# Kernel optimization log

Hardware: AMD Instinct MI355X
Metric: run time of the kernel (lower is better)

The kernel has to match this reference:

```python
import jax, jax.numpy as jnp
import numpy as np

N, B, D, H, E = 1024, 8, 768, 8, 16384
DH = D // H
EPS = 1e-5


def setup_inputs() -> dict:
    key = jax.random.key(0)
    ks = jax.random.split(key, 12)
    s = 0.02
    return {
        "x": jax.random.normal(ks[0], (N, B, D), jnp.float32),
        "edge_index": jax.random.randint(ks[1], (B, 2, E), 0, N, jnp.int32),
        "gcn_W": jax.random.normal(ks[2], (D, D), jnp.float32) * s,
        "gcn_b": jnp.zeros((D,), jnp.float32),
        "in_proj_w": jax.random.normal(ks[3], (3 * D, D), jnp.float32) * s,
        "in_proj_b": jnp.zeros((3 * D,), jnp.float32),
        "out_proj_w": jax.random.normal(ks[4], (D, D), jnp.float32) * s,
        "out_proj_b": jnp.zeros((D,), jnp.float32),
        "gate_w": jax.random.normal(ks[5], (D, 2 * D), jnp.float32) * s,
        "gate_b": jnp.zeros((D,), jnp.float32),
        "ln_g": jnp.ones((D,), jnp.float32),
        "ln_b": jnp.zeros((D,), jnp.float32),
    }


def _gcn(xb, edge_index, gcn_W, gcn_b):
    # xb: [B, N, D] node features; edge_index: [B, 2, E]
    h = xb @ gcn_W.T  # linear first, as in PyG GCNConv
    loops = jnp.arange(N, dtype=edge_index.dtype)

    def agg(h_b, ei_b):
        src = jnp.concatenate([ei_b[0], loops])  # add self-loops
        dst = jnp.concatenate([ei_b[1], loops])
        deg = jax.ops.segment_sum(jnp.ones_like(src, h_b.dtype), dst, num_segments=N)
        dinv = jnp.where(deg > 0, jax.lax.rsqrt(deg), 0.0)
        norm = dinv[src] * dinv[dst]  # symmetric normalization
        msg = norm[:, None] * h_b[src]
        return jax.ops.segment_sum(msg, dst, num_segments=N)

    return jax.vmap(agg)(h, edge_index) + gcn_b  # [B, N, D]


def _mha(x, in_proj_w, in_proj_b, out_proj_w, out_proj_b):
    # x: [N, B, D] (seq-first, as nn.MultiheadAttention default)
    qkv = x @ in_proj_w.T + in_proj_b  # [N, B, 3D]
    q, k, v = jnp.split(qkv, 3, axis=-1)

    def heads(t):  # [N, B, D] -> [B, H, N, DH]
        return t.reshape(N, B, H, DH).transpose(1, 2, 0, 3)

    q, k, v = heads(q), heads(k), heads(v)
    scores = jnp.einsum("bhqd,bhkd->bhqk", q, k) / jnp.sqrt(jnp.float32(DH))
    attn = jax.nn.softmax(scores, axis=-1)
    ctx = jnp.einsum("bhqk,bhkd->bhqd", attn, v)  # [B, H, N, DH]
    ctx = ctx.transpose(2, 0, 1, 3).reshape(N, B, D)
    return ctx @ out_proj_w.T + out_proj_b


def _layernorm(x, g, b):
    mu = jnp.mean(x, axis=-1, keepdims=True)
    var = jnp.mean(jnp.square(x - mu), axis=-1, keepdims=True)
    return (x - mu) * jax.lax.rsqrt(var + EPS) * g + b


def reference(x, edge_index, gcn_W, gcn_b, in_proj_w, in_proj_b,
              out_proj_w, out_proj_b, gate_w, gate_b, ln_g, ln_b):
    xb = x.transpose(1, 0, 2)  # [B, N, D]
    gcn_out = _gcn(xb, edge_index, gcn_W, gcn_b).transpose(1, 0, 2)  # [N, B, D]
    attn_out = _mha(x, in_proj_w, in_proj_b, out_proj_w, out_proj_b)  # [N, B, D]
    combined = jnp.concatenate([gcn_out, attn_out], axis=-1)
    gate = jax.nn.sigmoid(combined @ gate_w.T + gate_b)
    fused = gate * gcn_out + (1.0 - gate) * attn_out
    return _layernorm(fused + x, ln_g, ln_b)
```

## Files before the change

### kernel.cpp

```cpp
#include <hip/hip_runtime.h>


typedef __attribute__((ext_vector_type(8))) short b16x8;
typedef __attribute__((ext_vector_type(4))) float f32x4;

using gu32 = __attribute__((address_space(1))) const unsigned int;
using lu32 = __attribute__((address_space(3))) unsigned int;

constexpr int N  = 1024;
constexpr int B  = 8;
constexpr int D  = 768;
constexpr int H  = 8;
constexpr int DH = 96;
constexpr int E  = 16384;
constexpr int M  = N * B;
constexpr float LN_EPS = 1e-5f;

#define DEV static __device__ __forceinline__

DEV unsigned short f2b(float f) {
  unsigned u = __float_as_uint(f);
  u += 0x7fffu + ((u >> 16) & 1u);
  return (unsigned short)(u >> 16);
}
DEV float b2f(unsigned short h) { return __uint_as_float(((unsigned)h) << 16); }

__global__ void cast_f2b_kernel(const float* __restrict__ in,
                                unsigned short* __restrict__ out, int n4) {
  int i = blockIdx.x * 256 + threadIdx.x;
  if (i < n4) {
    float4 v = ((const float4*)in)[i];
    ushort4 o;
    o.x = f2b(v.x); o.y = f2b(v.y); o.z = f2b(v.z); o.w = f2b(v.w);
    ((ushort4*)out)[i] = o;
  }
}

__global__ void zero_i32_kernel(int* __restrict__ p, int n) {
  int i = blockIdx.x * 256 + threadIdx.x;
  if (i < n) p[i] = 0;
}

__global__ void edge_count_kernel(const int* __restrict__ ei, int* __restrict__ cnt) {
  int i = blockIdx.x * 256 + threadIdx.x;
  int b = i >> 14, e = i & (E - 1);
  int dst = ei[(b << 15) + E + e];
  atomicAdd(&cnt[(b << 10) + dst], 1);
}

__global__ __launch_bounds__(1024) void scan_offs_kernel(
    const int* __restrict__ cnt, int* __restrict__ offs,
    int* __restrict__ cursor, float* __restrict__ dinv) {
  __shared__ int buf[1024];
  const int b = blockIdx.x, i = threadIdx.x, g = (b << 10) + i;
  const int c = cnt[g];
  buf[i] = c;
  __syncthreads();
  for (int off = 1; off < 1024; off <<= 1) {
    int t = (i >= off) ? buf[i - off] : 0;
    __syncthreads();
    buf[i] += t;
    __syncthreads();
  }
  const int excl = buf[i] - c;
  offs[g] = excl;
  cursor[g] = excl;
  dinv[g] = rsqrtf((float)(c + 1));
}

__global__ void edge_fill_kernel(const int* __restrict__ ei,
                                 int* __restrict__ cursor, int* __restrict__ elist) {
  int i = blockIdx.x * 256 + threadIdx.x;
  int b = i >> 14, e = i & (E - 1);
  int src = ei[(b << 15) + e];
  int dst = ei[(b << 15) + E + e];
  int slot = atomicAdd(&cursor[(b << 10) + dst], 1);
  elist[(b << 14) + slot] = src;
}

constexpr int EPI_FUSED = 0;
constexpr int EPI_ATTN  = 1;
constexpr int EPI_GATE  = 2;

template <int EPI, int BN, int K>
__global__ __launch_bounds__(256) void gemm_bt(
    const unsigned short* __restrict__ A, const unsigned short* __restrict__ W,
    const float* __restrict__ bias,
    void* __restrict__ p0, void* __restrict__ p1, void* __restrict__ p2,
    void* __restrict__ p3) {
  constexpr int NW = BN / 32;
  constexpr int NT = K / 32;
  __shared__ __align__(16) unsigned short sA[2][128][32];
  __shared__ __align__(16) unsigned short sB[2][BN][32];
  const int tid = threadIdx.x;
  const int lane = tid & 63, wid = tid >> 6;
  const int wm = wid >> 1, wn = wid & 1;
  const int m0 = blockIdx.y * 128, n0 = blockIdx.x * BN;
  const int l15 = lane & 15, lhi = lane >> 4;
  const int srow = lane >> 2, scol = (lane & 3) * 8;

  f32x4 acc[4][NW] = {};

  const unsigned short* pa = A + ((size_t)(m0 + wid * 32 + srow)) * K + scol;
  const unsigned short* pb = W + ((size_t)(n0 + wid * (BN / 4) + srow)) * K + scol;

  auto stage = [&](int buf) {
    __builtin_amdgcn_global_load_lds((gu32*)pa, (lu32*)&sA[buf][wid * 32][0], 16, 0, 0);
    __builtin_amdgcn_global_load_lds((gu32*)(pa + 16 * K),
                                     (lu32*)&sA[buf][wid * 32 + 16][0], 16, 0, 0);
    __builtin_amdgcn_global_load_lds((gu32*)pb, (lu32*)&sB[buf][wid * (BN / 4)][0], 16, 0, 0);
    if constexpr (BN == 128)
      __builtin_amdgcn_global_load_lds((gu32*)(pb + 16 * K),
                                       (lu32*)&sB[buf][wid * 32 + 16][0], 16, 0, 0);
    pa += 32; pb += 32;
  };

  stage(0);
  int cur = 0;
  for (int kt = 0; kt < NT; ++kt) {
    if (kt + 1 < NT) {
      stage(cur ^ 1);
      if constexpr (BN == 128) asm volatile("s_waitcnt vmcnt(4)" ::: "memory");
      else                     asm volatile("s_waitcnt vmcnt(3)" ::: "memory");
    } else {
      asm volatile("s_waitcnt vmcnt(0)" ::: "memory");
    }
    __builtin_amdgcn_s_barrier();
    __builtin_amdgcn_sched_barrier(0);

    b16x8 af[4], bfr[NW];
#pragma unroll
    for (int i = 0; i < 4; ++i)
      af[i] = *(const b16x8*)&sA[cur][wm * 64 + i * 16 + l15][lhi * 8];
#pragma unroll
    for (int j = 0; j < NW; ++j)
      bfr[j] = *(const b16x8*)&sB[cur][wn * (BN / 2) + j * 16 + l15][lhi * 8];
#pragma unroll
    for (int i = 0; i < 4; ++i)
#pragma unroll
      for (int j = 0; j < NW; ++j)
        acc[i][j] = __builtin_amdgcn_mfma_f32_16x16x32_bf16(af[i], bfr[j], acc[i][j], 0, 0, 0);

    __builtin_amdgcn_sched_barrier(0);
    __builtin_amdgcn_s_barrier();
    cur ^= 1;
  }

#pragma unroll
  for (int i = 0; i < 4; ++i) {
#pragma unroll
    for (int j = 0; j < NW; ++j) {
      const int c = n0 + wn * (BN / 2) + j * 16 + l15;
      float bv;
      if constexpr (EPI == EPI_FUSED) bv = (c < 768) ? 0.0f : bias[c - 768];
      else bv = bias[c];
#pragma unroll
      for (int g = 0; g < 4; ++g) {
        const int r = m0 + wm * 64 + i * 16 + lhi * 4 + g;
        float v = acc[i][j][g] + bv;
        if constexpr (EPI == EPI_FUSED) {
          const int n = r >> 3, b = r & 7;
          if (c < 768) {
            ((unsigned short*)p0)[((size_t)((b << 10) + n)) * 768 + c] = f2b(v);
          } else {
            const int cc2 = c - 768;
            const int sec = cc2 / 768, cc = cc2 - sec * 768;
            const int hd = cc / 96, dh = cc - hd * 96;
            unsigned short* dst =
                (sec == 0) ? (unsigned short*)p1
                           : (sec == 1 ? (unsigned short*)p2 : (unsigned short*)p3);
            size_t idx;
            if (sec < 2) idx = ((size_t)((b * 8 + hd) * 1024 + n)) * 96 + dh;
            else         idx = ((size_t)((b * 8 + hd) * 96 + dh)) * 1024 + n;
            dst[idx] = f2b(v);
          }
        } else if constexpr (EPI == EPI_ATTN) {
          ((float*)p1)[(size_t)r * 768 + c] = v;
          ((unsigned short*)p0)[(size_t)r * 1536 + 768 + c] = f2b(v);
        } else {
          ((float*)p1)[(size_t)r * 768 + c] = 1.0f / (1.0f + __expf(-v));
        }
      }
    }
  }
}

__global__ __launch_bounds__(256) void attn_kernel(
    const unsigned short* __restrict__ qb, const unsigned short* __restrict__ kb,
    const unsigned short* __restrict__ vb, unsigned short* __restrict__ ctx) {
  __shared__ __align__(16) unsigned short sK[64][104];
  __shared__ __align__(16) unsigned short sV[96][72];
  __shared__ __align__(16) unsigned short sP[4][16][72];
  const int tid = threadIdx.x, lane = tid & 63, wid = tid >> 6;
  const int l15 = lane & 15, lhi = lane >> 4;
  const int bid = blockIdx.x;
  const int xcd = bid & 7, slot = bid >> 3;
  const int bh = xcd * 8 + (slot >> 4);
  const int q0 = (slot & 15) * 64;
  const float SCL = 0.14724445f;

  b16x8 qf[3];
  const size_t qbase = ((size_t)bh * 1024 + q0 + wid * 16 + l15) * 96 + lhi * 8;
#pragma unroll
  for (int ks = 0; ks < 3; ++ks) qf[ks] = *(const b16x8*)(qb + qbase + ks * 32);

  const int c0 = tid, c1 = 256 + tid, c2 = 512 + tid;
  const unsigned short* kp0 = kb + ((size_t)bh * 1024 + c0 / 12) * 96 + (c0 % 12) * 8;
  const unsigned short* kp1 = kb + ((size_t)bh * 1024 + c1 / 12) * 96 + (c1 % 12) * 8;
  const unsigned short* kp2 = kb + ((size_t)bh * 1024 + c2 / 12) * 96 + (c2 % 12) * 8;
  const unsigned short* vp0 = vb + ((size_t)bh * 96 + (c0 >> 3)) * 1024 + (c0 & 7) * 8;
  const unsigned short* vp1 = vb + ((size_t)bh * 96 + (c1 >> 3)) * 1024 + (c1 & 7) * 8;
  const unsigned short* vp2 = vb + ((size_t)bh * 96 + (c2 >> 3)) * 1024 + (c2 & 7) * 8;
  unsigned short* sk0 = &sK[c0 / 12][(c0 % 12) * 8];
  unsigned short* sk1 = &sK[c1 / 12][(c1 % 12) * 8];
  unsigned short* sk2 = &sK[c2 / 12][(c2 % 12) * 8];
  unsigned short* sv0 = &sV[c0 >> 3][(c0 & 7) * 8];
  unsigned short* sv1 = &sV[c1 >> 3][(c1 & 7) * 8];
  unsigned short* sv2 = &sV[c2 >> 3][(c2 & 7) * 8];

  uint4 k0 = *(const uint4*)kp0, k1 = *(const uint4*)kp1, k2 = *(const uint4*)kp2;
  uint4 v0 = *(const uint4*)vp0, v1 = *(const uint4*)vp1, v2 = *(const uint4*)vp2;

  f32x4 accO[6] = {};
  float ssum[4] = {0.f, 0.f, 0.f, 0.f};

  for (int kt = 0; kt < 16; ++kt) {
    __syncthreads();
    *(uint4*)sk0 = k0; *(uint4*)sk1 = k1; *(uint4*)sk2 = k2;
    *(uint4*)sv0 = v0; *(uint4*)sv1 = v1; *(uint4*)sv2 = v2;
    __syncthreads();
    if (kt < 15) {
      kp0 += 64 * 96; kp1 += 64 * 96; kp2 += 64 * 96;
      vp0 += 64;      vp1 += 64;      vp2 += 64;
      k0 = *(const uint4*)kp0; k1 = *(const uint4*)kp1; k2 = *(const uint4*)kp2;
      v0 = *(const uint4*)vp0; v1 = *(const uint4*)vp1; v2 = *(const uint4*)vp2;
    }

    f32x4 sf[4] = {};
#pragma unroll
    for (int f = 0; f < 4; ++f) {
#pragma unroll
      for (int ks = 0; ks < 3; ++ks) {
        b16x8 kf = *(const b16x8*)&sK[f * 16 + l15][ks * 32 + lhi * 8];
        sf[f] = __builtin_amdgcn_mfma_f32_16x16x32_bf16(qf[ks], kf, sf[f], 0, 0, 0);
      }
    }

#pragma unroll
    for (int g = 0; g < 4; ++g) {
#pragma unroll
      for (int f = 0; f < 4; ++f) {
        const float pv = exp2f(sf[f][g] * SCL);
        sP[wid][lhi * 4 + g][f * 16 + l15] = f2b(pv);
        ssum[g] += pv;
      }
    }

#pragma unroll
    for (int ks = 0; ks < 2; ++ks) {
      b16x8 pa = *(const b16x8*)&sP[wid][l15][ks * 32 + lhi * 8];
#pragma unroll
      for (int o = 0; o < 6; ++o) {
        b16x8 vf = *(const b16x8*)&sV[o * 16 + l15][ks * 32 + lhi * 8];
        accO[o] = __builtin_amdgcn_mfma_f32_16x16x32_bf16(pa, vf, accO[o], 0, 0, 0);
      }
    }
  }

#pragma unroll
  for (int g = 0; g < 4; ++g) {
#pragma unroll
    for (int msk = 1; msk < 16; msk <<= 1) ssum[g] += __shfl_xor(ssum[g], msk);
  }

  const int b = bh >> 3, hd = bh & 7;
  float rinv[4];
#pragma unroll
  for (int g = 0; g < 4; ++g) rinv[g] = 1.0f / ssum[g];
#pragma unroll
  for (int o = 0; o < 6; ++o)
#pragma unroll
    for (int g = 0; g < 4; ++g) {
      const int qrow = q0 + wid * 16 + lhi * 4 + g;
      ctx[((size_t)qrow * 8 + b) * 768 + hd * 96 + o * 16 + l15] =
          f2b(accO[o][g] * rinv[g]);
    }
}

__global__ __launch_bounds__(192) void gcn_agg_kernel(
    const unsigned short* __restrict__ h16,
    const int* __restrict__ cnt, const int* __restrict__ offs,
    const int* __restrict__ elist, const float* __restrict__ dinv,
    const float* __restrict__ gcn_b, float* __restrict__ gcn_f32,
    unsigned short* __restrict__ cat16) {
  const int bn = blockIdx.x;
  const int b = bn >> 10, n = bn & 1023;
  const int d = threadIdx.x * 4;
  const float dn = dinv[bn];
  const size_t hrow = (size_t)bn * 768;
  ushort4 hv = *(const ushort4*)(h16 + hrow + d);
  float a0 = dn * dn * b2f(hv.x), a1 = dn * dn * b2f(hv.y);
  float a2 = dn * dn * b2f(hv.z), a3 = dn * dn * b2f(hv.w);
  const int st = offs[bn], cv = cnt[bn];
  const int* ep = elist + (b << 14) + st;
  int src = (cv > 0) ? ep[0] : 0;
  for (int i = 0; i < cv; ++i) {
    const int nsrc = (i + 1 < cv) ? ep[i + 1] : 0;
    const float nv = dinv[(b << 10) + src] * dn;
    const ushort4 sv = *(const ushort4*)(h16 + ((size_t)((b << 10) + src)) * 768 + d);
    a0 += nv * b2f(sv.x); a1 += nv * b2f(sv.y);
    a2 += nv * b2f(sv.z); a3 += nv * b2f(sv.w);
    src = nsrc;
  }
  const float4 bb = *(const float4*)(gcn_b + d);
  a0 += bb.x; a1 += bb.y; a2 += bb.z; a3 += bb.w;
  *(float4*)(gcn_f32 + hrow + d) = make_float4(a0, a1, a2, a3);
  const size_t crow = ((size_t)n * 8 + b) * 1536;
  ushort4 co; co.x = f2b(a0); co.y = f2b(a1); co.z = f2b(a2); co.w = f2b(a3);
  *(ushort4*)(cat16 + crow + d) = co;
}

__global__ __launch_bounds__(192) void ln_fuse_kernel(
    const float* __restrict__ gate, const float* __restrict__ gcn,
    const float* __restrict__ attn, const float* __restrict__ x,
    const float* __restrict__ lng, const float* __restrict__ lnb,
    float* __restrict__ out) {
  const int r = blockIdx.x;
  const int t = threadIdx.x, lane = t & 63, wid = t >> 6;
  const int b = r & 7, n = r >> 3;
  const int d = t * 4;
  const size_t xrow = (size_t)r * 768;
  const size_t grow = (size_t)((b << 10) + n) * 768;
  const float4 gv = *(const float4*)(gate + xrow + d);
  const float4 cv = *(const float4*)(gcn + grow + d);
  const float4 av = *(const float4*)(attn + xrow + d);
  const float4 xv = *(const float4*)(x + xrow + d);
  float f0 = gv.x * cv.x + (1.f - gv.x) * av.x + xv.x;
  float f1 = gv.y * cv.y + (1.f - gv.y) * av.y + xv.y;
  float f2 = gv.z * cv.z + (1.f - gv.z) * av.z + xv.z;
  float f3 = gv.w * cv.w + (1.f - gv.w) * av.w + xv.w;
  float s1 = f0 + f1 + f2 + f3;
  float s2 = f0 * f0 + f1 * f1 + f2 * f2 + f3 * f3;
#pragma unroll
  for (int msk = 1; msk < 64; msk <<= 1) {
    s1 += __shfl_xor(s1, msk);
    s2 += __shfl_xor(s2, msk);
  }
  __shared__ float p1[3], p2[3];
  if (lane == 0) { p1[wid] = s1; p2[wid] = s2; }
  __syncthreads();
  s1 = p1[0] + p1[1] + p1[2];
  s2 = p2[0] + p2[1] + p2[2];
  const float mu = s1 * (1.f / 768.f);
  float var = s2 * (1.f / 768.f) - mu * mu;
  var = fmaxf(var, 0.f);
  const float rstd = rsqrtf(var + LN_EPS);
  const float4 lg = *(const float4*)(lng + d);
  const float4 lb = *(const float4*)(lnb + d);
  float4 o;
  o.x = (f0 - mu) * rstd * lg.x + lb.x;
  o.y = (f1 - mu) * rstd * lg.y + lb.y;
  o.z = (f2 - mu) * rstd * lg.z + lb.z;
  o.w = (f3 - mu) * rstd * lg.w + lb.w;
  *(float4*)(out + xrow + d) = o;
}

extern "C" void kernel_launch(void* const* d_in, const int* in_sizes, int n_in,
                              void* d_out, int out_size, void* d_ws, size_t ws_size,
                              hipStream_t stream) {
  const float* x     = (const float*)d_in[0];
  const int*   ei    = (const int*)d_in[1];
  const float* gcnW  = (const float*)d_in[2];
  const float* gcnb  = (const float*)d_in[3];
  const float* ipw   = (const float*)d_in[4];
  const float* ipb   = (const float*)d_in[5];
  const float* opw   = (const float*)d_in[6];
  const float* opb   = (const float*)d_in[7];
  const float* gw    = (const float*)d_in[8];
  const float* gb    = (const float*)d_in[9];
  const float* lng   = (const float*)d_in[10];
  const float* lnb   = (const float*)d_in[11];
  float* out = (float*)d_out;

  char* p = (char*)d_ws;
  auto alloc = [&](size_t bytes) { void* q = p; p += (bytes + 255) & ~(size_t)255; return q; };

  unsigned short* xb16  = (unsigned short*)alloc((size_t)M * 768 * 2);
  unsigned short* wcat  = (unsigned short*)alloc((size_t)3072 * 768 * 2);
  unsigned short* wout  = (unsigned short*)alloc((size_t)768 * 768 * 2);
  unsigned short* wgate = (unsigned short*)alloc((size_t)768 * 1536 * 2);
  unsigned short* qb    = (unsigned short*)alloc((size_t)B * H * N * DH * 2);
  unsigned short* kb    = (unsigned short*)alloc((size_t)B * H * N * DH * 2);
  unsigned short* vb    = (unsigned short*)alloc((size_t)B * H * DH * N * 2);
  unsigned short* h16   = (unsigned short*)alloc((size_t)M * 768 * 2);
  unsigned short* cat16 = (unsigned short*)alloc((size_t)M * 1536 * 2);
  float* gcnf           = (float*)alloc((size_t)M * 768 * 4);
  int* cnt    = (int*)alloc(8192 * 4);
  int* offs   = (int*)alloc(8192 * 4);
  int* cursor = (int*)alloc(8192 * 4);
  float* dinv = (float*)alloc(8192 * 4);
  int* elist  = (int*)alloc((size_t)B * E * 4);

  unsigned short* ctx16 = xb16;
  float* gatef = (float*)qb;
  float* attnf = (float*)vb;

  cast_f2b_kernel<<<(M * 768 / 4 + 255) / 256, 256, 0, stream>>>(x, xb16, M * 768 / 4);
  cast_f2b_kernel<<<(768 * 768 / 4 + 255) / 256, 256, 0, stream>>>(gcnW, wcat, 768 * 768 / 4);
  cast_f2b_kernel<<<(2304 * 768 / 4 + 255) / 256, 256, 0, stream>>>(
      ipw, wcat + (size_t)768 * 768, 2304 * 768 / 4);
  cast_f2b_kernel<<<(768 * 768 / 4 + 255) / 256, 256, 0, stream>>>(opw, wout, 768 * 768 / 4);
  cast_f2b_kernel<<<(768 * 1536 / 4 + 255) / 256, 256, 0, stream>>>(gw, wgate, 768 * 1536 / 4);

  zero_i32_kernel<<<32, 256, 0, stream>>>(cnt, 8192);
  edge_count_kernel<<<(B * E) / 256, 256, 0, stream>>>(ei, cnt);
  scan_offs_kernel<<<8, 1024, 0, stream>>>(cnt, offs, cursor, dinv);
  edge_fill_kernel<<<(B * E) / 256, 256, 0, stream>>>(ei, cursor, elist);

  gemm_bt<EPI_FUSED, 128, 768><<<dim3(24, 64), 256, 0, stream>>>(
      xb16, wcat, ipb, (void*)h16, (void*)qb, (void*)kb, (void*)vb);
  attn_kernel<<<1024, 256, 0, stream>>>(qb, kb, vb, ctx16);
  gcn_agg_kernel<<<8192, 192, 0, stream>>>(h16, cnt, offs, elist, dinv, gcnb,
                                           gcnf, cat16);
  gemm_bt<EPI_ATTN, 64, 768><<<dim3(12, 64), 256, 0, stream>>>(
      ctx16, wout, opb, (void*)cat16, (void*)attnf, nullptr, nullptr);
  gemm_bt<EPI_GATE, 64, 1536><<<dim3(12, 64), 256, 0, stream>>>(
      cat16, wgate, gb, nullptr, (void*)gatef, nullptr, nullptr);

  ln_fuse_kernel<<<8192, 192, 0, stream>>>(gatef, gcnf, attnf, x, lng, lnb, out);
}
```

Before: 285.1 us.

## Replace fused QKV/GCN GEMM with 256x256-tile, 8-wave pipelined kernel

Adds a dedicated 256x256-tile, 512-thread GEMM for the fused GCN-linear plus QKV projection (M=8192, N=3072, K=768). It uses K=64 double-buffered LDS stages and splits each stage into four MFMA phases, with async global-to-LDS loads interleaved between phases and s_setprio raised around the MFMA blocks. The larger tile raises arithmetic intensity and cuts redundant global traffic compared with the old 128x128 tiles. The cost is heavy register use (128 accumulator floats per lane) and only 384 blocks, which may leave the GPU's CUs unevenly loaded.

```diff
diff --git a/kernel.cpp b/kernel.cpp
--- a/kernel.cpp
+++ b/kernel.cpp
@@ -17,6 +17,7 @@
 constexpr float LN_EPS = 1e-5f;
 
 #define DEV static __device__ __forceinline__
+#define GLOAD(SRC, DST) __builtin_amdgcn_global_load_lds((gu32*)(SRC), (lu32*)(DST), 16, 0, 0)
 
 DEV unsigned short f2b(float f) {
   unsigned u = __float_as_uint(f);
@@ -78,7 +79,166 @@
   elist[(b << 14) + slot] = src;
 }
 
-constexpr int EPI_FUSED = 0;
+__global__ __launch_bounds__(512, 2) void gemm_fused256(
+    const unsigned short* __restrict__ A, const unsigned short* __restrict__ W,
+    const float* __restrict__ bias,
+    void* __restrict__ p0, void* __restrict__ p1, void* __restrict__ p2,
+    void* __restrict__ p3) {
+  __shared__ __align__(16) unsigned short sA[2][2][256][32];
+  __shared__ __align__(16) unsigned short sB[2][2][256][32];
+  const int tid = threadIdx.x;
+  const int lane = tid & 63, wid = tid >> 6;
+  const int wm = wid >> 2, wn = wid & 3;
+  const int m0 = blockIdx.y * 256, n0 = blockIdx.x * 256;
+  const int l15 = lane & 15, lhi = lane >> 4;
+
+  f32x4 acc[8][4] = {};
+
+  const unsigned short* pa = A + ((size_t)(m0 + (tid >> 2))) * 768 + (tid & 3) * 8;
+  const unsigned short* pb = W + ((size_t)(n0 + (tid >> 2))) * 768 + (tid & 3) * 8;
+  constexpr size_t RSTRIDE = (size_t)128 * 768;
+
+  GLOAD(pb,                 &sB[0][0][wid * 16][0]);
+  GLOAD(pb + RSTRIDE,       &sB[0][0][128 + wid * 16][0]);
+  GLOAD(pa,                 &sA[0][0][wid * 16][0]);
+  GLOAD(pa + RSTRIDE,       &sA[0][0][128 + wid * 16][0]);
+  GLOAD(pb + 32,            &sB[0][1][wid * 16][0]);
+  GLOAD(pb + 32 + RSTRIDE,  &sB[0][1][128 + wid * 16][0]);
+  GLOAD(pa + 32,            &sA[0][1][wid * 16][0]);
+  GLOAD(pa + 32 + RSTRIDE,  &sA[0][1][128 + wid * 16][0]);
+  asm volatile("s_waitcnt vmcnt(4)" ::: "memory");
+  __builtin_amdgcn_s_barrier();
+
+  for (int t = 0; t < 12; ++t) {
+    const int p = t & 1;
+    const bool stg = (t < 11);
+    const int kn = (t + 1) * 64;
+    b16x8 af[4], bf[4];
+
+#pragma unroll
+    for (int cf = 0; cf < 4; ++cf)
+      bf[cf] = *(const b16x8*)&sB[p][0][wn * 64 + cf * 16 + l15][lhi * 8];
+#pragma unroll
+    for (int rf = 0; rf < 4; ++rf)
+      af[rf] = *(const b16x8*)&sA[p][0][wm * 128 + rf * 16 + l15][lhi * 8];
+    if (stg) {
+      GLOAD(pb + kn,           &sB[p ^ 1][0][wid * 16][0]);
+      GLOAD(pb + kn + RSTRIDE, &sB[p ^ 1][0][128 + wid * 16][0]);
+    }
+    __builtin_amdgcn_sched_barrier(0);
+    __builtin_amdgcn_s_barrier();
+    asm volatile("s_waitcnt lgkmcnt(0)" ::: "memory");
+    __builtin_amdgcn_sched_barrier(0);
+    __builtin_amdgcn_s_setprio(1);
+#pragma unroll
+    for (int rf = 0; rf < 4; ++rf)
+#pragma unroll
+      for (int cf = 0; cf < 4; ++cf)
+        acc[rf][cf] = __builtin_amdgcn_mfma_f32_16x16x32_bf16(af[rf], bf[cf], acc[rf][cf], 0, 0, 0);
+    __builtin_amdgcn_s_setprio(0);
+    __builtin_amdgcn_sched_barrier(0);
+    __builtin_amdgcn_s_barrier();
+
+#pragma unroll
+    for (int rf = 0; rf < 4; ++rf)
+      af[rf] = *(const b16x8*)&sA[p][0][wm * 128 + 64 + rf * 16 + l15][lhi * 8];
+    if (stg) {
+      GLOAD(pa + kn,           &sA[p ^ 1][0][wid * 16][0]);
+      GLOAD(pa + kn + RSTRIDE, &sA[p ^ 1][0][128 + wid * 16][0]);
+    }
+    __builtin_amdgcn_sched_barrier(0);
+    if (stg) asm volatile("s_waitcnt vmcnt(4)" ::: "memory");
+    else     asm volatile("s_waitcnt vmcnt(0)" ::: "memory");
+    __builtin_amdgcn_s_barrier();
+    asm volatile("s_waitcnt lgkmcnt(0)" ::: "memory");
+    __builtin_amdgcn_sched_barrier(0);
+    __builtin_amdgcn_s_setprio(1);
+#pragma unroll
+    for (int rf = 0; rf < 4; ++rf)
+#pragma unroll
+      for (int cf = 0; cf < 4; ++cf)
+        acc[4 + rf][cf] = __builtin_amdgcn_mfma_f32_16x16x32_bf16(af[rf], bf[cf], acc[4 + rf][cf], 0, 0, 0);
+    __builtin_amdgcn_s_setprio(0);
+    __builtin_amdgcn_sched_barrier(0);
+    __builtin_amdgcn_s_barrier();
+
+#pragma unroll
+    for (int cf = 0; cf < 4; ++cf)
+      bf[cf] = *(const b16x8*)&sB[p][1][wn * 64 + cf * 16 + l15][lhi * 8];
+#pragma unroll
+    for (int rf = 0; rf < 4; ++rf)
+      af[rf] = *(const b16x8*)&sA[p][1][wm * 128 + rf * 16 + l15][lhi * 8];
+    if (stg) {
+      GLOAD(pb + kn + 32,           &sB[p ^ 1][1][wid * 16][0]);
+      GLOAD(pb + kn + 32 + RSTRIDE, &sB[p ^ 1][1][128 + wid * 16][0]);
+    }
+    __builtin_amdgcn_sched_barrier(0);
+    __builtin_amdgcn_s_barrier();
+    asm volatile("s_waitcnt lgkmcnt(0)" ::: "memory");
+    __builtin_amdgcn_sched_barrier(0);
+    __builtin_amdgcn_s_setprio(1);
+#pragma unroll
+    for (int rf = 0; rf < 4; ++rf)
+#pragma unroll
+      for (int cf = 0; cf < 4; ++cf)
+        acc[rf][cf] = __builtin_amdgcn_mfma_f32_16x16x32_bf16(af[rf], bf[cf], acc[rf][cf], 0, 0, 0);
+    __builtin_amdgcn_s_setprio(0);
+    __builtin_amdgcn_sched_barrier(0);
+    __builtin_amdgcn_s_barrier();
+
+#pragma unroll
+    for (int rf = 0; rf < 4; ++rf)
+      af[rf] = *(const b16x8*)&sA[p][1][wm * 128 + 64 + rf * 16 + l15][lhi * 8];
+    if (stg) {
+      GLOAD(pa + kn + 32,           &sA[p ^ 1][1][wid * 16][0]);
+      GLOAD(pa + kn + 32 + RSTRIDE, &sA[p ^ 1][1][128 + wid * 16][0]);
+    }
+    __builtin_amdgcn_sched_barrier(0);
+    if (stg) asm volatile("s_waitcnt vmcnt(4)" ::: "memory");
+    __builtin_amdgcn_s_barrier();
+    asm volatile("s_waitcnt lgkmcnt(0)" ::: "memory");
+    __builtin_amdgcn_sched_barrier(0);
+    __builtin_amdgcn_s_setprio(1);
+#pragma unroll
+    for (int rf = 0; rf < 4; ++rf)
+#pragma unroll
+      for (int cf = 0; cf < 4; ++cf)
+        acc[4 + rf][cf] = __builtin_amdgcn_mfma_f32_16x16x32_bf16(af[rf], bf[cf], acc[4 + rf][cf], 0, 0, 0);
+    __builtin_amdgcn_s_setprio(0);
+    __builtin_amdgcn_sched_barrier(0);
+    __builtin_amdgcn_s_barrier();
+  }
+
+#pragma unroll
+  for (int rg = 0; rg < 8; ++rg) {
+#pragma unroll
+    for (int cf = 0; cf < 4; ++cf) {
+      const int c = n0 + wn * 64 + cf * 16 + l15;
+      const float bv = (c < 768) ? 0.0f : bias[c - 768];
+#pragma unroll
+      for (int g = 0; g < 4; ++g) {
+        const int r = m0 + wm * 128 + rg * 16 + lhi * 4 + g;
+        float v = acc[rg][cf][g] + bv;
+        const int n = r >> 3, b = r & 7;
+        if (c < 768) {
+          ((unsigned short*)p0)[((size_t)((b << 10) + n)) * 768 + c] = f2b(v);
+        } else {
+          const int cc2 = c - 768;
+          const int sec = cc2 / 768, cc = cc2 - sec * 768;
+          const int hd = cc / 96, dh = cc - hd * 96;
+          unsigned short* dst =
+              (sec == 0) ? (unsigned short*)p1
+                         : (sec == 1 ? (unsigned short*)p2 : (unsigned short*)p3);
+          size_t idx;
+          if (sec < 2) idx = ((size_t)((b * 8 + hd) * 1024 + n)) * 96 + dh;
+          else         idx = ((size_t)((b * 8 + hd) * 96 + dh)) * 1024 + n;
+          dst[idx] = f2b(v);
+        }
+      }
+    }
+  }
+}
+
 constexpr int EPI_ATTN  = 1;
 constexpr int EPI_GATE  = 2;
 
@@ -86,8 +246,7 @@
 __global__ __launch_bounds__(256) void gemm_bt(
     const unsigned short* __restrict__ A, const unsigned short* __restrict__ W,
     const float* __restrict__ bias,
-    void* __restrict__ p0, void* __restrict__ p1, void* __restrict__ p2,
-    void* __restrict__ p3) {
+    void* __restrict__ p0, void* __restrict__ p1) {
   constexpr int NW = BN / 32;
   constexpr int NT = K / 32;
   __shared__ __align__(16) unsigned short sA[2][128][32];
@@ -105,13 +264,10 @@
   const unsigned short* pb = W + ((size_t)(n0 + wid * (BN / 4) + srow)) * K + scol;
 
   auto stage = [&](int buf) {
-    __builtin_amdgcn_global_load_lds((gu32*)pa, (lu32*)&sA[buf][wid * 32][0], 16, 0, 0);
-    __builtin_amdgcn_global_load_lds((gu32*)(pa + 16 * K),
-                                     (lu32*)&sA[buf][wid * 32 + 16][0], 16, 0, 0);
-    __builtin_amdgcn_global_load_lds((gu32*)pb, (lu32*)&sB[buf][wid * (BN / 4)][0], 16, 0, 0);
-    if constexpr (BN == 128)
-      __builtin_amdgcn_global_load_lds((gu32*)(pb + 16 * K),
-                                       (lu32*)&sB[buf][wid * 32 + 16][0], 16, 0, 0);
+    GLOAD(pa,          &sA[buf][wid * 32][0]);
+    GLOAD(pa + 16 * K, &sA[buf][wid * 32 + 16][0]);
+    GLOAD(pb,          &sB[buf][wid * (BN / 4)][0]);
+    if constexpr (BN == 128) GLOAD(pb + 16 * K, &sB[buf][wid * 32 + 16][0]);
     pa += 32; pb += 32;
   };
 
@@ -151,30 +307,12 @@
 #pragma unroll
     for (int j = 0; j < NW; ++j) {
       const int c = n0 + wn * (BN / 2) + j * 16 + l15;
-      float bv;
-      if constexpr (EPI == EPI_FUSED) bv = (c < 768) ? 0.0f : bias[c - 768];
-      else bv = bias[c];
+      const float bv = bias[c];
 #pragma unroll
       for (int g = 0; g < 4; ++g) {
         const int r = m0 + wm * 64 + i * 16 + lhi * 4 + g;
         float v = acc[i][j][g] + bv;
-        if constexpr (EPI == EPI_FUSED) {
-          const int n = r >> 3, b = r & 7;
-          if (c < 768) {
-            ((unsigned short*)p0)[((size_t)((b << 10) + n)) * 768 + c] = f2b(v);
-          } else {
-            const int cc2 = c - 768;
-            const int sec = cc2 / 768, cc = cc2 - sec * 768;
-            const int hd = cc / 96, dh = cc - hd * 96;
-            unsigned short* dst =
-                (sec == 0) ? (unsigned short*)p1
-                           : (sec == 1 ? (unsigned short*)p2 : (unsigned short*)p3);
-            size_t idx;
-            if (sec < 2) idx = ((size_t)((b * 8 + hd) * 1024 + n)) * 96 + dh;
-            else         idx = ((size_t)((b * 8 + hd) * 96 + dh)) * 1024 + n;
-            dst[idx] = f2b(v);
-          }
-        } else if constexpr (EPI == EPI_ATTN) {
+        if constexpr (EPI == EPI_ATTN) {
           ((float*)p1)[(size_t)r * 768 + c] = v;
           ((unsigned short*)p0)[(size_t)r * 1536 + 768 + c] = f2b(v);
         } else {
@@ -417,15 +555,15 @@
   scan_offs_kernel<<<8, 1024, 0, stream>>>(cnt, offs, cursor, dinv);
   edge_fill_kernel<<<(B * E) / 256, 256, 0, stream>>>(ei, cursor, elist);
 
-  gemm_bt<EPI_FUSED, 128, 768><<<dim3(24, 64), 256, 0, stream>>>(
+  gemm_fused256<<<dim3(12, 32), 512, 0, stream>>>(
       xb16, wcat, ipb, (void*)h16, (void*)qb, (void*)kb, (void*)vb);
   attn_kernel<<<1024, 256, 0, stream>>>(qb, kb, vb, ctx16);
   gcn_agg_kernel<<<8192, 192, 0, stream>>>(h16, cnt, offs, elist, dinv, gcnb,
                                            gcnf, cat16);
   gemm_bt<EPI_ATTN, 64, 768><<<dim3(12, 64), 256, 0, stream>>>(
-      ctx16, wout, opb, (void*)cat16, (void*)attnf, nullptr, nullptr);
+      ctx16, wout, opb, (void*)cat16, (void*)attnf);
   gemm_bt<EPI_GATE, 64, 1536><<<dim3(12, 64), 256, 0, stream>>>(
-      cat16, wgate, gb, nullptr, (void*)gatef, nullptr, nullptr);
+      cat16, wgate, gb, nullptr, (void*)gatef);
 
   ln_fuse_kernel<<<8192, 192, 0, stream>>>(gatef, gcnf, attnf, x, lng, lnb, out);
 }
```

Measured after the change: 300.9 us. 1.06x slower.

## Drop fp32 intermediates, read bf16 cat buffer in LN, merge cast kernels

Applied to the files above, without the earlier changes.

Removes the fp32 gcn and attention output buffers and stores the gate as bf16, so the final layernorm kernel reads the bf16 GCN and attention values from the concatenated buffer instead. This cuts global memory traffic in the gcn_agg, out-proj, gate and LN stages. The five cast launches become one kernel, and the GCN aggregation loop is unrolled by two so two gathers are in flight at once. The cost is lower precision in the gate and fused values (bf16 instead of fp32), which could affect accuracy.

```diff
diff --git a/kernel.cpp b/kernel.cpp
--- a/kernel.cpp
+++ b/kernel.cpp
@@ -17,6 +17,7 @@
 constexpr float LN_EPS = 1e-5f;
 
 #define DEV static __device__ __forceinline__
+#define GLOAD(SRC, DST) __builtin_amdgcn_global_load_lds((gu32*)(SRC), (lu32*)(DST), 16, 0, 0)
 
 DEV unsigned short f2b(float f) {
   unsigned u = __float_as_uint(f);
@@ -25,15 +26,29 @@
 }
 DEV float b2f(unsigned short h) { return __uint_as_float(((unsigned)h) << 16); }
 
-__global__ void cast_f2b_kernel(const float* __restrict__ in,
-                                unsigned short* __restrict__ out, int n4) {
-  int i = blockIdx.x * 256 + threadIdx.x;
-  if (i < n4) {
-    float4 v = ((const float4*)in)[i];
-    ushort4 o;
-    o.x = f2b(v.x); o.y = f2b(v.y); o.z = f2b(v.z); o.w = f2b(v.w);
-    ((ushort4*)out)[i] = o;
-  }
+constexpr int CS0 = 1572864;
+constexpr int CS1 = CS0 + 147456;
+constexpr int CS2 = CS1 + 442368;
+constexpr int CS3 = CS2 + 147456;
+constexpr int CS4 = CS3 + 294912;
+__global__ void cast_all_kernel(
+    const float* __restrict__ x, const float* __restrict__ gcnW,
+    const float* __restrict__ ipw, const float* __restrict__ opw,
+    const float* __restrict__ gw,
+    unsigned short* __restrict__ xb16, unsigned short* __restrict__ wcat,
+    unsigned short* __restrict__ wout, unsigned short* __restrict__ wgate) {
+  const int i = blockIdx.x * 256 + threadIdx.x;
+  if (i >= CS4) return;
+  const float* in; unsigned short* out; int off;
+  if (i < CS0)      { in = x;    out = xb16;           off = i; }
+  else if (i < CS1) { in = gcnW; out = wcat;           off = i - CS0; }
+  else if (i < CS2) { in = ipw;  out = wcat + 589824;  off = i - CS1; }
+  else if (i < CS3) { in = opw;  out = wout;           off = i - CS2; }
+  else              { in = gw;   out = wgate;          off = i - CS3; }
+  float4 v = ((const float4*)in)[off];
+  ushort4 o;
+  o.x = f2b(v.x); o.y = f2b(v.y); o.z = f2b(v.z); o.w = f2b(v.w);
+  ((ushort4*)out)[off] = o;
 }
 
 __global__ void zero_i32_kernel(int* __restrict__ p, int n) {
@@ -105,13 +120,10 @@
   const unsigned short* pb = W + ((size_t)(n0 + wid * (BN / 4) + srow)) * K + scol;
 
   auto stage = [&](int buf) {
-    __builtin_amdgcn_global_load_lds((gu32*)pa, (lu32*)&sA[buf][wid * 32][0], 16, 0, 0);
-    __builtin_amdgcn_global_load_lds((gu32*)(pa + 16 * K),
-                                     (lu32*)&sA[buf][wid * 32 + 16][0], 16, 0, 0);
-    __builtin_amdgcn_global_load_lds((gu32*)pb, (lu32*)&sB[buf][wid * (BN / 4)][0], 16, 0, 0);
-    if constexpr (BN == 128)
-      __builtin_amdgcn_global_load_lds((gu32*)(pb + 16 * K),
-                                       (lu32*)&sB[buf][wid * 32 + 16][0], 16, 0, 0);
+    GLOAD(pa,          &sA[buf][wid * 32][0]);
+    GLOAD(pa + 16 * K, &sA[buf][wid * 32 + 16][0]);
+    GLOAD(pb,          &sB[buf][wid * (BN / 4)][0]);
+    if constexpr (BN == 128) GLOAD(pb + 16 * K, &sB[buf][wid * 32 + 16][0]);
     pa += 32; pb += 32;
   };
 
@@ -175,10 +187,10 @@
             dst[idx] = f2b(v);
           }
         } else if constexpr (EPI == EPI_ATTN) {
-          ((float*)p1)[(size_t)r * 768 + c] = v;
           ((unsigned short*)p0)[(size_t)r * 1536 + 768 + c] = f2b(v);
         } else {
-          ((float*)p1)[(size_t)r * 768 + c] = 1.0f / (1.0f + __expf(-v));
+          ((unsigned short*)p0)[(size_t)r * 768 + c] =
+              f2b(1.0f / (1.0f + __expf(-v)));
         }
       }
     }
@@ -291,8 +303,7 @@
     const unsigned short* __restrict__ h16,
     const int* __restrict__ cnt, const int* __restrict__ offs,
     const int* __restrict__ elist, const float* __restrict__ dinv,
-    const float* __restrict__ gcn_b, float* __restrict__ gcn_f32,
-    unsigned short* __restrict__ cat16) {
+    const float* __restrict__ gcn_b, unsigned short* __restrict__ cat16) {
   const int bn = blockIdx.x;
   const int b = bn >> 10, n = bn & 1023;
   const int d = threadIdx.x * 4;
@@ -303,42 +314,52 @@
   float a2 = dn * dn * b2f(hv.z), a3 = dn * dn * b2f(hv.w);
   const int st = offs[bn], cv = cnt[bn];
   const int* ep = elist + (b << 14) + st;
-  int src = (cv > 0) ? ep[0] : 0;
-  for (int i = 0; i < cv; ++i) {
-    const int nsrc = (i + 1 < cv) ? ep[i + 1] : 0;
-    const float nv = dinv[(b << 10) + src] * dn;
-    const ushort4 sv = *(const ushort4*)(h16 + ((size_t)((b << 10) + src)) * 768 + d);
-    a0 += nv * b2f(sv.x); a1 += nv * b2f(sv.y);
-    a2 += nv * b2f(sv.z); a3 += nv * b2f(sv.w);
-    src = nsrc;
+  int i = 0;
+  for (; i + 2 <= cv; i += 2) {
+    const int s0 = ep[i], s1 = ep[i + 1];
+    const float nv0 = dinv[(b << 10) + s0] * dn;
+    const float nv1 = dinv[(b << 10) + s1] * dn;
+    const ushort4 r0 = *(const ushort4*)(h16 + ((size_t)((b << 10) + s0)) * 768 + d);
+    const ushort4 r1 = *(const ushort4*)(h16 + ((size_t)((b << 10) + s1)) * 768 + d);
+    a0 += nv0 * b2f(r0.x) + nv1 * b2f(r1.x);
+    a1 += nv0 * b2f(r0.y) + nv1 * b2f(r1.y);
+    a2 += nv0 * b2f(r0.z) + nv1 * b2f(r1.z);
+    a3 += nv0 * b2f(r0.w) + nv1 * b2f(r1.w);
+  }
+  if (i < cv) {
+    const int s0 = ep[i];
+    const float nv0 = dinv[(b << 10) + s0] * dn;
+    const ushort4 r0 = *(const ushort4*)(h16 + ((size_t)((b << 10) + s0)) * 768 + d);
+    a0 += nv0 * b2f(r0.x); a1 += nv0 * b2f(r0.y);
+    a2 += nv0 * b2f(r0.z); a3 += nv0 * b2f(r0.w);
   }
   const float4 bb = *(const float4*)(gcn_b + d);
   a0 += bb.x; a1 += bb.y; a2 += bb.z; a3 += bb.w;
-  *(float4*)(gcn_f32 + hrow + d) = make_float4(a0, a1, a2, a3);
   const size_t crow = ((size_t)n * 8 + b) * 1536;
   ushort4 co; co.x = f2b(a0); co.y = f2b(a1); co.z = f2b(a2); co.w = f2b(a3);
   *(ushort4*)(cat16 + crow + d) = co;
 }
 
 __global__ __launch_bounds__(192) void ln_fuse_kernel(
-    const float* __restrict__ gate, const float* __restrict__ gcn,
-    const float* __restrict__ attn, const float* __restrict__ x,
+    const unsigned short* __restrict__ gate16,
+    const unsigned short* __restrict__ cat16,
+    const float* __restrict__ x,
     const float* __restrict__ lng, const float* __restrict__ lnb,
     float* __restrict__ out) {
   const int r = blockIdx.x;
   const int t = threadIdx.x, lane = t & 63, wid = t >> 6;
-  const int b = r & 7, n = r >> 3;
   const int d = t * 4;
   const size_t xrow = (size_t)r * 768;
-  const size_t grow = (size_t)((b << 10) + n) * 768;
-  const float4 gv = *(const float4*)(gate + xrow + d);
-  const float4 cv = *(const float4*)(gcn + grow + d);
-  const float4 av = *(const float4*)(attn + xrow + d);
+  const size_t crow = (size_t)r * 1536;
+  const ushort4 gv = *(const ushort4*)(gate16 + xrow + d);
+  const ushort4 cv = *(const ushort4*)(cat16 + crow + d);
+  const ushort4 av = *(const ushort4*)(cat16 + crow + 768 + d);
   const float4 xv = *(const float4*)(x + xrow + d);
-  float f0 = gv.x * cv.x + (1.f - gv.x) * av.x + xv.x;
-  float f1 = gv.y * cv.y + (1.f - gv.y) * av.y + xv.y;
-  float f2 = gv.z * cv.z + (1.f - gv.z) * av.z + xv.z;
-  float f3 = gv.w * cv.w + (1.f - gv.w) * av.w + xv.w;
+  const float g0 = b2f(gv.x), g1 = b2f(gv.y), g2 = b2f(gv.z), g3 = b2f(gv.w);
+  float f0 = g0 * b2f(cv.x) + (1.f - g0) * b2f(av.x) + xv.x;
+  float f1 = g1 * b2f(cv.y) + (1.f - g1) * b2f(av.y) + xv.y;
+  float f2 = g2 * b2f(cv.z) + (1.f - g2) * b2f(av.z) + xv.z;
+  float f3 = g3 * b2f(cv.w) + (1.f - g3) * b2f(av.w) + xv.w;
   float s1 = f0 + f1 + f2 + f3;
   float s2 = f0 * f0 + f1 * f1 + f2 * f2 + f3 * f3;
 #pragma unroll
@@ -394,23 +415,17 @@
   unsigned short* vb    = (unsigned short*)alloc((size_t)B * H * DH * N * 2);
   unsigned short* h16   = (unsigned short*)alloc((size_t)M * 768 * 2);
   unsigned short* cat16 = (unsigned short*)alloc((size_t)M * 1536 * 2);
-  float* gcnf           = (float*)alloc((size_t)M * 768 * 4);
   int* cnt    = (int*)alloc(8192 * 4);
   int* offs   = (int*)alloc(8192 * 4);
   int* cursor = (int*)alloc(8192 * 4);
   float* dinv = (float*)alloc(8192 * 4);
   int* elist  = (int*)alloc((size_t)B * E * 4);
 
-  unsigned short* ctx16 = xb16;
-  float* gatef = (float*)qb;
-  float* attnf = (float*)vb;
-
-  cast_f2b_kernel<<<(M * 768 / 4 + 255) / 256, 256, 0, stream>>>(x, xb16, M * 768 / 4);
-  cast_f2b_kernel<<<(768 * 768 / 4 + 255) / 256, 256, 0, stream>>>(gcnW, wcat, 768 * 768 / 4);
-  cast_f2b_kernel<<<(2304 * 768 / 4 + 255) / 256, 256, 0, stream>>>(
-      ipw, wcat + (size_t)768 * 768, 2304 * 768 / 4);
-  cast_f2b_kernel<<<(768 * 768 / 4 + 255) / 256, 256, 0, stream>>>(opw, wout, 768 * 768 / 4);
-  cast_f2b_kernel<<<(768 * 1536 / 4 + 255) / 256, 256, 0, stream>>>(gw, wgate, 768 * 1536 / 4);
+  unsigned short* ctx16  = xb16;
+  unsigned short* gate16 = qb;
+
+  cast_all_kernel<<<(CS4 + 255) / 256, 256, 0, stream>>>(
+      x, gcnW, ipw, opw, gw, xb16, wcat, wout, wgate);
 
   zero_i32_kernel<<<32, 256, 0, stream>>>(cnt, 8192);
   edge_count_kernel<<<(B * E) / 256, 256, 0, stream>>>(ei, cnt);
@@ -420,12 +435,11 @@
   gemm_bt<EPI_FUSED, 128, 768><<<dim3(24, 64), 256, 0, stream>>>(
       xb16, wcat, ipb, (void*)h16, (void*)qb, (void*)kb, (void*)vb);
   attn_kernel<<<1024, 256, 0, stream>>>(qb, kb, vb, ctx16);
-  gcn_agg_kernel<<<8192, 192, 0, stream>>>(h16, cnt, offs, elist, dinv, gcnb,
-                                           gcnf, cat16);
+  gcn_agg_kernel<<<8192, 192, 0, stream>>>(h16, cnt, offs, elist, dinv, gcnb, cat16);
   gemm_bt<EPI_ATTN, 64, 768><<<dim3(12, 64), 256, 0, stream>>>(
-      ctx16, wout, opb, (void*)cat16, (void*)attnf, nullptr, nullptr);
+      ctx16, wout, opb, (void*)cat16, nullptr, nullptr, nullptr);
   gemm_bt<EPI_GATE, 64, 1536><<<dim3(12, 64), 256, 0, stream>>>(
-      cat16, wgate, gb, nullptr, (void*)gatef, nullptr, nullptr);
-
-  ln_fuse_kernel<<<8192, 192, 0, stream>>>(gatef, gcnf, attnf, x, lng, lnb, out);
-}
+      cat16, wgate, gb, (void*)gate16, nullptr, nullptr, nullptr);
+
+  ln_fuse_kernel<<<8192, 192, 0, stream>>>(gate16, cat16, x, lng, lnb, out);
+}
```

New measurement: 263.5 us. 1.08x faster.
